# Performance work log

Measured on AMD Instinct MI355X. Metric: run time of the kernel, lower is better.

The kernel has to match this reference:

```python
import jax, jax.numpy as jnp
import numpy as np

PLANES = 128
SCALE = float(np.sqrt(PLANES))
TEMP = 0.05


def _maxpool2x2(x):
    # x: [B, C, H, W] -> [B, C, H//2, W//2]
    return jax.lax.reduce_window(x, -jnp.inf, jax.lax.max,
                                 (1, 1, 2, 2), (1, 1, 2, 2), 'VALID')


def _conv1x1(x, w, b=None):
    # x: [B, Cin, H, W], w: [Cout, Cin]
    y = jnp.einsum('bchw,oc->bohw', x, w)
    if b is not None:
        y = y + b[None, :, None, None]
    return y


def setup_inputs() -> dict:
    key = jax.random.key(0)
    ks = jax.random.split(key, 9)
    B, C, H, W = 8, 512, 64, 64
    std = 0.01  # init.normal_(w, 0, 0.01)
    x = jax.random.normal(ks[0], (B, C, H, W), dtype=jnp.float32)
    wq = jax.random.normal(ks[1], (PLANES, C), dtype=jnp.float32) * std
    bq = jnp.zeros((PLANES,), dtype=jnp.float32)
    wk = jax.random.normal(ks[2], (PLANES, C), dtype=jnp.float32) * std
    bk = jnp.zeros((PLANES,), dtype=jnp.float32)
    wv = jax.random.normal(ks[3], (C, C), dtype=jnp.float32) * std  # no bias (use_out=False)
    wm = jax.random.normal(ks[4], (1, C), dtype=jnp.float32) * std
    bm = jnp.zeros((1,), dtype=jnp.float32)
    # torch inits gamma to zero; use a nonzero value so the attention path matters
    gamma = jax.random.normal(ks[5], (1,), dtype=jnp.float32)
    return {'x': x, 'wq': wq, 'bq': bq, 'wk': wk, 'bk': bk,
            'wv': wv, 'wm': wm, 'bm': bm, 'gamma': gamma}


def reference(x, wq, bq, wk, bk, wv, wm, bm, gamma):
    B, C, H, W = x.shape
    xd = _maxpool2x2(x)                                   # [B,C,H/2,W/2]
    Hm, Wm = xd.shape[2], xd.shape[3]
    N, M = H * W, Hm * Wm
    q = _conv1x1(x, wq, bq).reshape(B, PLANES, N)         # [B,P,N]
    k = _conv1x1(xd, wk, bk).reshape(B, PLANES, M)        # [B,P,M]
    v = _conv1x1(xd, wv).reshape(B, C, M)                 # [B,C,M]
    # 'channel' whitening: subtract per-channel spatial mean
    q = q - q.mean(axis=2, keepdims=True)
    k = k - k.mean(axis=2, keepdims=True)
    sim = jnp.einsum('bpn,bpm->bnm', q, k) / (SCALE * TEMP)  # [B,N,M]
    sim = jax.nn.softmax(sim, axis=2)
    out_sim = jnp.einsum('bnm,bcm->bcn', sim, v).reshape(B, C, H, W)
    out_sim = gamma[0] * out_sim
    # global-context branch (with_gc, no 2fc)
    mask = _conv1x1(xd, wm, bm).reshape(B, M)             # [B,M]
    mask = jax.nn.softmax(mask, axis=1)
    out_gc = jnp.einsum('bcm,bm->bc', v, mask)[:, :, None, None]  # [B,C,1,1]
    return out_sim + out_gc + x
```

## Files before the change

kernel.cpp:

```cpp
#include <hip/hip_runtime.h>

typedef float f32x4 __attribute__((ext_vector_type(4)));
typedef short bf16x8 __attribute__((ext_vector_type(8)));
typedef short s16x4 __attribute__((ext_vector_type(4)));
typedef unsigned short u16;

#define B_ 8
#define C_ 512
#define N_ 4096
#define M_ 1024
#define P_ 128
#define A2C 2.5506631384888954f
#define B2C 23.083120654223414f

#define MFMA __builtin_amdgcn_mfma_f32_16x16x32_bf16

__device__ __forceinline__ u16 f2b(float f) {
  unsigned u = __float_as_uint(f);
  u += 0x7fffu + ((u >> 16) & 1u);
  return (u16)(u >> 16);
}
__device__ __forceinline__ float b2f(u16 h) {
  return __uint_as_float(((unsigned)h) << 16);
}
__device__ __forceinline__ float waveRedSum(float v) {
#pragma unroll
  for (int off = 32; off > 0; off >>= 1) v += __shfl_xor(v, off);
  return v;
}
__device__ __forceinline__ void gload_lds16(const u16* g, u16* l) {
  __builtin_amdgcn_global_load_lds(
      (const __attribute__((address_space(1))) void*)g,
      (__attribute__((address_space(3))) void*)l, 16, 0, 0);
}

__global__ __launch_bounds__(256) void prep_tx(const float* __restrict__ x,
                                               u16* __restrict__ xt,
                                               u16* __restrict__ xdt,
                                               float* __restrict__ meanx,
                                               float* __restrict__ meanxd) {
  const int bid = blockIdx.x;
  const int b = bid >> 8, ct = (bid >> 5) & 7, hp = bid & 31;
  const int t = threadIdx.x;
  const int lane = t & 63, wid = t >> 6;
  __shared__ float xs[64 * 133];
  __shared__ float part[4][64];
  const float* xb = x + ((size_t)(b * 512 + ct * 64) * 4096) + hp * 128;
#pragma unroll
  for (int it = 0; it < 32; ++it) {
    int c = it * 2 + (t >> 7);
    int n = t & 127;
    xs[c * 133 + n] = xb[(size_t)c * 4096 + n];
  }
  __syncthreads();
  {
    int c = t >> 2, qq = t & 3;
    float s = 0;
#pragma unroll
    for (int j = 0; j < 32; ++j) s += xs[c * 133 + qq * 32 + j];
    s += __shfl_xor(s, 1);
    s += __shfl_xor(s, 2);
    if (qq == 0) atomicAdd(&meanx[b * 512 + ct * 64 + c], s * (1.f / 4096.f));
  }
#pragma unroll
  for (int it = 0; it < 16; ++it) {
    int n = it * 8 + (t >> 5), cp = t & 31;
    float lo = xs[(2 * cp) * 133 + n], hi = xs[(2 * cp + 1) * 133 + n];
    unsigned u = (unsigned)f2b(lo) | ((unsigned)f2b(hi) << 16);
    *(unsigned*)(xt + (((size_t)b * 4096) + hp * 128 + n) * 512 + ct * 64 + 2 * cp) = u;
  }
  float s0 = 0, s1 = 0;
  const int cp = t & 31;
#pragma unroll
  for (int it = 0; it < 4; ++it) {
    int wm = it * 8 + (t >> 5);
    int c0 = 2 * cp;
    float a = fmaxf(fmaxf(xs[c0 * 133 + 2 * wm], xs[c0 * 133 + 2 * wm + 1]),
                    fmaxf(xs[c0 * 133 + 64 + 2 * wm], xs[c0 * 133 + 64 + 2 * wm + 1]));
    float d = fmaxf(fmaxf(xs[(c0 + 1) * 133 + 2 * wm], xs[(c0 + 1) * 133 + 2 * wm + 1]),
                    fmaxf(xs[(c0 + 1) * 133 + 64 + 2 * wm], xs[(c0 + 1) * 133 + 64 + 2 * wm + 1]));
    unsigned u = (unsigned)f2b(a) | ((unsigned)f2b(d) << 16);
    *(unsigned*)(xdt + (((size_t)b * 1024) + hp * 32 + wm) * 512 + ct * 64 + c0) = u;
    s0 += a; s1 += d;
  }
  s0 += __shfl_xor(s0, 32);
  s1 += __shfl_xor(s1, 32);
  if (lane < 32) { part[wid][2 * cp] = s0; part[wid][2 * cp + 1] = s1; }
  __syncthreads();
  if (t < 64)
    atomicAdd(&meanxd[b * 512 + ct * 64 + t],
              (part[0][t] + part[1][t] + part[2][t] + part[3][t]) * (1.f / 1024.f));
}

__global__ __launch_bounds__(256) void wcvt(const float* __restrict__ wq,
                                            const float* __restrict__ wk,
                                            const float* __restrict__ wv,
                                            const float* __restrict__ wm,
                                            const float* __restrict__ bm,
                                            const float* __restrict__ meanx,
                                            const float* __restrict__ meanxd,
                                            const u16* __restrict__ xdt,
                                            u16* __restrict__ wq_b,
                                            u16* __restrict__ wk_b,
                                            u16* __restrict__ wv_b,
                                            float* __restrict__ corr_q,
                                            float* __restrict__ corr_k,
                                            float* __restrict__ logits) {
  const int bid = blockIdx.x, t = threadIdx.x;
  if (bid < 1536) {
    int i = bid * 256 + t;
    if (i < 65536) wq_b[i] = f2b(wq[i]);
    else if (i < 131072) wk_b[i - 65536] = f2b(wk[i - 65536]);
    else wv_b[i - 131072] = f2b(wv[i - 131072]);
  } else if (bid < 1552) {
    int blk = bid - 1536, b = blk & 7, sel = blk >> 3;
    const float* w = sel ? wk : wq;
    const float* mn = (sel ? meanxd : meanx) + b * 512;
    int p = t >> 1, h = t & 1;
    const float* wr = w + p * 512 + h * 256;
    const float* mr = mn + h * 256;
    float s = 0;
#pragma unroll 8
    for (int c = 0; c < 256; ++c) s += wr[c] * mr[c];
    s += __shfl_xor(s, 1);
    if (h == 0) (sel ? corr_k : corr_q)[b * 128 + p] = s;
  } else {
    int blk = bid - 1552;
    int b = blk >> 8, mblk = blk & 255;
    int lane = t & 63, wv4 = t >> 6;
    int m = mblk * 4 + wv4;
    bf16x8 h8 = *(const bf16x8*)(xdt + ((size_t)b * 1024 + m) * 512 + lane * 8);
    const float* wmr = wm + lane * 8;
    float s = 0;
#pragma unroll
    for (int j = 0; j < 8; ++j) s += b2f((u16)h8[j]) * wmr[j];
    s = waveRedSum(s);
    if (lane == 0) logits[b * 1024 + m] = s + bm[0];
  }
}

template <int BR, int BC, bool TRANS, bool CORR>
__global__ __launch_bounds__(256) void gemm_bt(const u16* __restrict__ A,
                                               const u16* __restrict__ Bt,
                                               const float* __restrict__ corr,
                                               u16* __restrict__ outp,
                                               int Cout, int Ncols) {
  constexpr int WR = BR / 2, WC = BC / 2, ITR = WR / 16, ITC = WC / 16;
  constexpr int AFR = BR * 8 / 256, BFR = BC * 8 / 256;
  const int b = blockIdx.z;
  const int col0 = blockIdx.x * BC;
  const int row0 = blockIdx.y * BR;
  const int tid = threadIdx.x;
  const int lane = tid & 63, wid = tid >> 6;
  const int g = lane >> 4, c16 = lane & 15;
  const int wr = (wid >> 1) * WR, wc = (wid & 1) * WC;
  __shared__ __align__(16) u16 As[BR][72];
  __shared__ __align__(16) u16 Bs[BC][72];
  const u16* Bb = Bt + (size_t)b * Ncols * 512;
  f32x4 acc[ITR][ITC];
#pragma unroll
  for (int i = 0; i < ITR; ++i)
#pragma unroll
    for (int j = 0; j < ITC; ++j) acc[i][j] = (f32x4){0.f, 0.f, 0.f, 0.f};

  for (int k0 = 0; k0 < 512; k0 += 64) {
#pragma unroll
    for (int i = 0; i < AFR; ++i) {
      int f = tid + i * 256;
      int r = f >> 3, c8 = f & 7;
      *(bf16x8*)&As[r][c8 * 8] =
          *(const bf16x8*)(A + (size_t)(row0 + r) * 512 + k0 + c8 * 8);
    }
#pragma unroll
    for (int i = 0; i < BFR; ++i) {
      int f = tid + i * 256;
      int r = f >> 3, c8 = f & 7;
      *(bf16x8*)&Bs[r][c8 * 8] =
          *(const bf16x8*)(Bb + (size_t)(col0 + r) * 512 + k0 + c8 * 8);
    }
    __syncthreads();
#pragma unroll
    for (int kk = 0; kk < 2; ++kk) {
      bf16x8 bfr[ITC];
#pragma unroll
      for (int j = 0; j < ITC; ++j)
        bfr[j] = *(const bf16x8*)&Bs[wc + j * 16 + c16][kk * 32 + g * 8];
#pragma unroll
      for (int i = 0; i < ITR; ++i) {
        bf16x8 af = *(const bf16x8*)&As[wr + i * 16 + c16][kk * 32 + g * 8];
#pragma unroll
        for (int j = 0; j < ITC; ++j)
          acc[i][j] = MFMA(af, bfr[j], acc[i][j], 0, 0, 0);
      }
    }
    __syncthreads();
  }
  if (TRANS) {
#pragma unroll
    for (int i = 0; i < ITR; ++i)
#pragma unroll
      for (int j = 0; j < ITC; ++j) {
        int row = row0 + wr + i * 16 + g * 4;
        int col = col0 + wc + j * 16 + c16;
        s16x4 h;
#pragma unroll
        for (int r = 0; r < 4; ++r) {
          float val = acc[i][j][r];
          if (CORR) val -= corr[b * 128 + row + r];
          h[r] = (short)f2b(val);
        }
        *(s16x4*)(outp + ((size_t)b * Ncols + col) * Cout + row) = h;
      }
  } else {
#pragma unroll
    for (int i = 0; i < ITR; ++i)
#pragma unroll
      for (int j = 0; j < ITC; ++j) {
        int row = row0 + wr + i * 16 + g * 4;
        int col = col0 + wc + j * 16 + c16;
#pragma unroll
        for (int r = 0; r < 4; ++r)
          outp[((size_t)b * Cout + row + r) * Ncols + col] = f2b(acc[i][j][r]);
      }
  }
}

__global__ __launch_bounds__(256) void k_gc(const float* __restrict__ logits,
                                            const u16* __restrict__ v,
                                            float* __restrict__ gc) {
  const int b = blockIdx.x >> 4, cc = blockIdx.x & 15;
  const int tid = threadIdx.x;
  const int lane = tid & 63, wid = tid >> 6;
  __shared__ float pl[1024];
  __shared__ float r4[4];
  __shared__ float stot[2];
  float4 lv = *(const float4*)&logits[b * 1024 + tid * 4];
  float mx = fmaxf(fmaxf(lv.x, lv.y), fmaxf(lv.z, lv.w));
#pragma unroll
  for (int off = 32; off > 0; off >>= 1) mx = fmaxf(mx, __shfl_xor(mx, off));
  if (lane == 0) r4[wid] = mx;
  __syncthreads();
  if (tid == 0) stot[0] = fmaxf(fmaxf(r4[0], r4[1]), fmaxf(r4[2], r4[3]));
  __syncthreads();
  const float M = stot[0];
  float e0 = __expf(lv.x - M), e1 = __expf(lv.y - M);
  float e2 = __expf(lv.z - M), e3 = __expf(lv.w - M);
  pl[tid * 4 + 0] = e0; pl[tid * 4 + 1] = e1;
  pl[tid * 4 + 2] = e2; pl[tid * 4 + 3] = e3;
  float ps = waveRedSum((e0 + e1) + (e2 + e3));
  if (lane == 0) r4[wid] = ps;
  __syncthreads();
  if (tid == 0) stot[1] = 1.0f / (r4[0] + r4[1] + r4[2] + r4[3]);
  __syncthreads();
  const float inv = stot[1];
  const int c = cc * 32 + (tid >> 3), sub = tid & 7;
  const u16* vr = v + ((size_t)b * 512 + c) * 1024 + sub * 128;
  const float* plr = pl + sub * 128;
  float s = 0;
#pragma unroll
  for (int i = 0; i < 16; ++i) {
    bf16x8 h = *(const bf16x8*)(vr + i * 8);
#pragma unroll
    for (int j = 0; j < 8; ++j) s += b2f((u16)h[j]) * plr[i * 8 + j];
  }
  s += __shfl_xor(s, 1);
  s += __shfl_xor(s, 2);
  s += __shfl_xor(s, 4);
  if (sub == 0) gc[b * 512 + c] = s * inv;
}

__device__ __forceinline__ void s_phase(const bf16x8* kbf, const bf16x8 (&qf)[2][4],
                                        u16* PlBuf, int nA, int o,
                                        float& lp0, float& lp1) {
  f32x4 sv0 = (f32x4){0.f, 0.f, 0.f, 0.f};
  f32x4 sv1 = (f32x4){0.f, 0.f, 0.f, 0.f};
#pragma unroll
  for (int kf = 0; kf < 4; ++kf) {
    sv0 = MFMA(kbf[kf], qf[0][kf], sv0, 0, 0, 0);
    sv1 = MFMA(kbf[kf], qf[1][kf], sv1, 0, 0, 0);
  }
  float p00 = exp2f(fmaf(sv0[0], A2C, -B2C));
  float p01 = exp2f(fmaf(sv0[1], A2C, -B2C));
  float p02 = exp2f(fmaf(sv0[2], A2C, -B2C));
  float p03 = exp2f(fmaf(sv0[3], A2C, -B2C));
  float p10 = exp2f(fmaf(sv1[0], A2C, -B2C));
  float p11 = exp2f(fmaf(sv1[1], A2C, -B2C));
  float p12 = exp2f(fmaf(sv1[2], A2C, -B2C));
  float p13 = exp2f(fmaf(sv1[3], A2C, -B2C));
  lp0 += (p00 + p01) + (p02 + p03);
  lp1 += (p10 + p11) + (p12 + p13);
  uint2 w0, w1;
  w0.x = (unsigned)f2b(p00) | ((unsigned)f2b(p01) << 16);
  w0.y = (unsigned)f2b(p02) | ((unsigned)f2b(p03) << 16);
  w1.x = (unsigned)f2b(p10) | ((unsigned)f2b(p11) << 16);
  w1.y = (unsigned)f2b(p12) | ((unsigned)f2b(p13) << 16);
  *(uint2*)&PlBuf[nA * 64 + o] = w0;
  *(uint2*)&PlBuf[(nA + 16) * 64 + o] = w1;
}

__global__ __launch_bounds__(512, 2) void attn(const u16* __restrict__ q,
                                               const u16* __restrict__ kt,
                                               const u16* __restrict__ v,
                                               const float* __restrict__ gc,
                                               const float* __restrict__ x,
                                               const float* __restrict__ gamma,
                                               float* __restrict__ out) {
  extern __shared__ __align__(16) char smem[];
  u16* Vl = (u16*)smem;
  u16* Pl = (u16*)(smem + 131072);
  float* l_s = (float*)(smem + 147456);
  const int bid = blockIdx.x;
  const int b = bid & 7;
  const int n0 = (bid >> 3) * 64;
  const int tid = threadIdx.x;
  const int lane = tid & 63, wid = tid >> 6;
  const int g = lane >> 4, c16 = lane & 15;
  const int mb = wid & 3, nh = wid >> 2;
  const int xsw = (c16 & 7) << 3;
  const int nA = nh * 32 + c16;
  const int po = (mb * 16 + g * 4) ^ xsw;

  bf16x8 qf[2][4];
  {
    const u16* qr = q + ((size_t)b * N_ + n0 + nh * 32 + c16) * P_ + g * 8;
#pragma unroll
    for (int t = 0; t < 2; ++t)
#pragma unroll
      for (int kf = 0; kf < 4; ++kf)
        qf[t][kf] = *(const bf16x8*)(qr + t * 16 * P_ + kf * 32);
  }
  const u16* ktr = kt + ((size_t)b * M_ + mb * 16 + c16) * P_ + g * 8;
  bf16x8 kb[2][4];
#pragma unroll
  for (int kf = 0; kf < 4; ++kf) kb[0][kf] = *(const bf16x8*)(ktr + kf * 32);
#pragma unroll
  for (int kf = 0; kf < 4; ++kf) kb[1][kf] = *(const bf16x8*)(ktr + 64 * P_ + kf * 32);
  const u16* vst = v + ((size_t)b * C_ + wid * 64 + (lane >> 3)) * M_ +
                   ((lane & 7) ^ (lane >> 3)) * 8;
#pragma unroll
  for (int i = 0; i < 8; ++i)
    gload_lds16(vst + (size_t)i * 8 * M_, Vl + (wid * 8 + i) * 512);

  float lp0 = 0.f, lp1 = 0.f;
  s_phase(kb[0], qf, Pl, nA, po, lp0, lp1);

  f32x4 acc[4][4];
#pragma unroll
  for (int i = 0; i < 4; ++i)
#pragma unroll
    for (int j = 0; j < 4; ++j) acc[i][j] = (f32x4){0.f, 0.f, 0.f, 0.f};

#pragma unroll 2
  for (int s = 0; s < 16; ++s) {
    const int par = s & 1, nxt = par ^ 1;
    if (s < 14) {
      const size_t moff = (size_t)(s + 2) * 64 * P_;
#pragma unroll
      for (int kf = 0; kf < 4; ++kf)
        kb[par][kf] = *(const bf16x8*)(ktr + moff + kf * 32);
      asm volatile("s_waitcnt vmcnt(4) lgkmcnt(0)" ::: "memory");
    } else {
      asm volatile("s_waitcnt vmcnt(0) lgkmcnt(0)" ::: "memory");
    }
    __builtin_amdgcn_sched_barrier(0);
    __builtin_amdgcn_s_barrier();
    __builtin_amdgcn_sched_barrier(0);
    if (s < 15) {
      const int m1 = (s + 1) * 64;
#pragma unroll
      for (int i = 0; i < 8; ++i)
        gload_lds16(vst + m1 + (size_t)i * 8 * M_,
                    Vl + nxt * 32768 + (wid * 8 + i) * 512);
    }
    const u16* VlP = Vl + par * 32768;
    const u16* PlP = Pl + par * 4096;
#pragma unroll
    for (int kk = 0; kk < 2; ++kk) {
      bf16x8 pb[4];
#pragma unroll
      for (int nb = 0; nb < 4; ++nb)
        pb[nb] = *(const bf16x8*)&PlP[(nb * 16 + c16) * 64 + ((kk * 32 + g * 8) ^ xsw)];
#pragma unroll
      for (int cf = 0; cf < 4; ++cf) {
        bf16x8 va = *(const bf16x8*)&VlP[(wid * 64 + cf * 16 + c16) * 64 +
                                         ((kk * 32 + g * 8) ^ xsw)];
#pragma unroll
        for (int nb = 0; nb < 4; ++nb)
          acc[cf][nb] = MFMA(va, pb[nb], acc[cf][nb], 0, 0, 0);
      }
    }
    if (s < 15) s_phase(kb[nxt], qf, Pl + nxt * 4096, nA, po, lp0, lp1);
  }

  lp0 += __shfl_xor(lp0, 16); lp0 += __shfl_xor(lp0, 32);
  lp1 += __shfl_xor(lp1, 16); lp1 += __shfl_xor(lp1, 32);
  if (lane < 16) {
    l_s[mb * 64 + nh * 32 + lane] = lp0;
    l_s[mb * 64 + nh * 32 + 16 + lane] = lp1;
  }
  __syncthreads();
  float linv[4];
#pragma unroll
  for (int nb = 0; nb < 4; ++nb) {
    int n = nb * 16 + c16;
    linv[nb] = 1.0f / (l_s[n] + l_s[64 + n] + l_s[128 + n] + l_s[192 + n]);
  }
  const float gam = gamma[0];
#pragma unroll
  for (int cf = 0; cf < 4; ++cf) {
    const int c = wid * 64 + cf * 16 + g * 4;
    float gcv[4];
#pragma unroll
    for (int r = 0; r < 4; ++r) gcv[r] = gc[b * C_ + c + r];
#pragma unroll
    for (int nb = 0; nb < 4; ++nb) {
      const size_t idx0 = ((size_t)b * C_ + c) * (size_t)N_ + n0 + nb * 16 + c16;
#pragma unroll
      for (int r = 0; r < 4; ++r) {
        const size_t idx = idx0 + (size_t)r * N_;
        out[idx] = gam * acc[cf][nb][r] * linv[nb] + gcv[r] + x[idx];
      }
    }
  }
}

extern "C" void kernel_launch(void* const* d_in, const int* in_sizes, int n_in,
                              void* d_out, int out_size, void* d_ws, size_t ws_size,
                              hipStream_t stream) {
  const float* x     = (const float*)d_in[0];
  const float* wq    = (const float*)d_in[1];
  const float* wk    = (const float*)d_in[3];
  const float* wv    = (const float*)d_in[5];
  const float* wm    = (const float*)d_in[6];
  const float* bm    = (const float*)d_in[7];
  const float* gamma = (const float*)d_in[8];
  float* out = (float*)d_out;
  char* ws = (char*)d_ws;

  u16*   xt     = (u16*)(ws + 0);
  u16*   xdt    = (u16*)(ws + 33554432);
  u16*   q_ws   = (u16*)(ws + 41943040);
  u16*   kt_ws  = (u16*)(ws + 50331648);
  u16*   v_ws   = (u16*)(ws + 52428800);
  u16*   wq_b   = (u16*)(ws + 60817408);
  u16*   wk_b   = (u16*)(ws + 60948480);
  u16*   wv_b   = (u16*)(ws + 61079552);
  float* meanx  = (float*)(ws + 61603840);
  float* meanxd = (float*)(ws + 61620224);
  float* corr_q = (float*)(ws + 61636608);
  float* corr_k = (float*)(ws + 61640704);
  float* gc     = (float*)(ws + 61644800);
  float* logits = (float*)(ws + 61661184);

  hipMemsetAsync(ws + 61603840, 0, 32768, stream);
  prep_tx<<<dim3(2048), dim3(256), 0, stream>>>(x, xt, xdt, meanx, meanxd);
  wcvt<<<dim3(3600), dim3(256), 0, stream>>>(wq, wk, wv, wm, bm, meanx, meanxd,
                                             xdt, wq_b, wk_b, wv_b, corr_q,
                                             corr_k, logits);
  gemm_bt<128, 128, true, true><<<dim3(32, 1, B_), dim3(256), 0, stream>>>(
      wq_b, xt, corr_q, q_ws, 128, 4096);
  gemm_bt<128, 64, true, true><<<dim3(16, 1, B_), dim3(256), 0, stream>>>(
      wk_b, xdt, corr_k, kt_ws, 128, 1024);
  gemm_bt<128, 128, false, false><<<dim3(8, 4, B_), dim3(256), 0, stream>>>(
      wv_b, xdt, nullptr, v_ws, 512, 1024);
  k_gc<<<dim3(128), dim3(256), 0, stream>>>(logits, v_ws, gc);

  hipFuncSetAttribute((const void*)attn,
                      hipFuncAttributeMaxDynamicSharedMemorySize, 148480);
  attn<<<dim3(512), dim3(512), 148480, stream>>>(q_ws, kt_ws, v_ws, gc, x,
                                                 gamma, out);
}
```

Baseline: 255.2 us.

## Fuse mask logits into prep, merge projection GEMMs, single-buffer attention LDS

Computes the global-context mask logits inside the pooling prep kernel via shuffle reductions and atomics, removing a separate pass over xdt. The three projection GEMMs are merged into one launch with a uniform 128x64 tile. The attention kernel drops double-buffered V/P LDS staging for a single buffer, halving shared memory so more blocks can be resident (launch bounds raised to 4), at the cost of an extra barrier per step and less load/compute overlap. The logits no longer add bm, which is dropped because a constant bias cancels in the softmax.

```diff
diff --git a/kernel.cpp b/kernel.cpp
--- a/kernel.cpp
+++ b/kernel.cpp
@@ -35,10 +35,12 @@
 }
 
 __global__ __launch_bounds__(256) void prep_tx(const float* __restrict__ x,
+                                               const float* __restrict__ wm,
                                                u16* __restrict__ xt,
                                                u16* __restrict__ xdt,
                                                float* __restrict__ meanx,
-                                               float* __restrict__ meanxd) {
+                                               float* __restrict__ meanxd,
+                                               float* __restrict__ logits) {
   const int bid = blockIdx.x;
   const int b = bid >> 8, ct = (bid >> 5) & 7, hp = bid & 31;
   const int t = threadIdx.x;
@@ -64,24 +66,30 @@
   }
 #pragma unroll
   for (int it = 0; it < 16; ++it) {
-    int n = it * 8 + (t >> 5), cp = t & 31;
-    float lo = xs[(2 * cp) * 133 + n], hi = xs[(2 * cp + 1) * 133 + n];
+    int n = it * 8 + (t >> 5), cp2 = t & 31;
+    float lo = xs[(2 * cp2) * 133 + n], hi = xs[(2 * cp2 + 1) * 133 + n];
     unsigned u = (unsigned)f2b(lo) | ((unsigned)f2b(hi) << 16);
-    *(unsigned*)(xt + (((size_t)b * 4096) + hp * 128 + n) * 512 + ct * 64 + 2 * cp) = u;
-  }
+    *(unsigned*)(xt + (((size_t)b * 4096) + hp * 128 + n) * 512 + ct * 64 + 2 * cp2) = u;
+  }
+  const int cp = t & 31;
+  const float wm0 = wm[ct * 64 + 2 * cp], wm1 = wm[ct * 64 + 2 * cp + 1];
   float s0 = 0, s1 = 0;
-  const int cp = t & 31;
 #pragma unroll
   for (int it = 0; it < 4; ++it) {
-    int wm = it * 8 + (t >> 5);
+    int wmi = it * 8 + (t >> 5);
     int c0 = 2 * cp;
-    float a = fmaxf(fmaxf(xs[c0 * 133 + 2 * wm], xs[c0 * 133 + 2 * wm + 1]),
-                    fmaxf(xs[c0 * 133 + 64 + 2 * wm], xs[c0 * 133 + 64 + 2 * wm + 1]));
-    float d = fmaxf(fmaxf(xs[(c0 + 1) * 133 + 2 * wm], xs[(c0 + 1) * 133 + 2 * wm + 1]),
-                    fmaxf(xs[(c0 + 1) * 133 + 64 + 2 * wm], xs[(c0 + 1) * 133 + 64 + 2 * wm + 1]));
+    float a = fmaxf(fmaxf(xs[c0 * 133 + 2 * wmi], xs[c0 * 133 + 2 * wmi + 1]),
+                    fmaxf(xs[c0 * 133 + 64 + 2 * wmi], xs[c0 * 133 + 64 + 2 * wmi + 1]));
+    float d = fmaxf(fmaxf(xs[(c0 + 1) * 133 + 2 * wmi], xs[(c0 + 1) * 133 + 2 * wmi + 1]),
+                    fmaxf(xs[(c0 + 1) * 133 + 64 + 2 * wmi], xs[(c0 + 1) * 133 + 64 + 2 * wmi + 1]));
     unsigned u = (unsigned)f2b(a) | ((unsigned)f2b(d) << 16);
-    *(unsigned*)(xdt + (((size_t)b * 1024) + hp * 32 + wm) * 512 + ct * 64 + c0) = u;
+    *(unsigned*)(xdt + (((size_t)b * 1024) + hp * 32 + wmi) * 512 + ct * 64 + c0) = u;
     s0 += a; s1 += d;
+    float lg = wm0 * a + wm1 * d;
+    lg += __shfl_xor(lg, 1);  lg += __shfl_xor(lg, 2);
+    lg += __shfl_xor(lg, 4);  lg += __shfl_xor(lg, 8);
+    lg += __shfl_xor(lg, 16);
+    if (cp == 0) atomicAdd(&logits[b * 1024 + hp * 32 + wmi], lg);
   }
   s0 += __shfl_xor(s0, 32);
   s1 += __shfl_xor(s1, 32);
@@ -95,24 +103,20 @@
 __global__ __launch_bounds__(256) void wcvt(const float* __restrict__ wq,
                                             const float* __restrict__ wk,
                                             const float* __restrict__ wv,
-                                            const float* __restrict__ wm,
-                                            const float* __restrict__ bm,
                                             const float* __restrict__ meanx,
                                             const float* __restrict__ meanxd,
-                                            const u16* __restrict__ xdt,
                                             u16* __restrict__ wq_b,
                                             u16* __restrict__ wk_b,
                                             u16* __restrict__ wv_b,
                                             float* __restrict__ corr_q,
-                                            float* __restrict__ corr_k,
-                                            float* __restrict__ logits) {
+                                            float* __restrict__ corr_k) {
   const int bid = blockIdx.x, t = threadIdx.x;
   if (bid < 1536) {
     int i = bid * 256 + t;
     if (i < 65536) wq_b[i] = f2b(wq[i]);
     else if (i < 131072) wk_b[i - 65536] = f2b(wk[i - 65536]);
     else wv_b[i - 131072] = f2b(wv[i - 131072]);
-  } else if (bid < 1552) {
+  } else {
     int blk = bid - 1536, b = blk & 7, sel = blk >> 3;
     const float* w = sel ? wk : wq;
     const float* mn = (sel ? meanxd : meanx) + b * 512;
@@ -124,38 +128,24 @@
     for (int c = 0; c < 256; ++c) s += wr[c] * mr[c];
     s += __shfl_xor(s, 1);
     if (h == 0) (sel ? corr_k : corr_q)[b * 128 + p] = s;
-  } else {
-    int blk = bid - 1552;
-    int b = blk >> 8, mblk = blk & 255;
-    int lane = t & 63, wv4 = t >> 6;
-    int m = mblk * 4 + wv4;
-    bf16x8 h8 = *(const bf16x8*)(xdt + ((size_t)b * 1024 + m) * 512 + lane * 8);
-    const float* wmr = wm + lane * 8;
-    float s = 0;
-#pragma unroll
-    for (int j = 0; j < 8; ++j) s += b2f((u16)h8[j]) * wmr[j];
-    s = waveRedSum(s);
-    if (lane == 0) logits[b * 1024 + m] = s + bm[0];
   }
 }
 
 template <int BR, int BC, bool TRANS, bool CORR>
-__global__ __launch_bounds__(256) void gemm_bt(const u16* __restrict__ A,
-                                               const u16* __restrict__ Bt,
-                                               const float* __restrict__ corr,
-                                               u16* __restrict__ outp,
-                                               int Cout, int Ncols) {
+__device__ __forceinline__ void gemm_body(const u16* __restrict__ A,
+                                          const u16* __restrict__ Bt,
+                                          const float* __restrict__ corr,
+                                          u16* __restrict__ outp,
+                                          int Cout, int Ncols,
+                                          int bx, int by, int b,
+                                          u16 (*As)[72], u16 (*Bs)[72]) {
   constexpr int WR = BR / 2, WC = BC / 2, ITR = WR / 16, ITC = WC / 16;
   constexpr int AFR = BR * 8 / 256, BFR = BC * 8 / 256;
-  const int b = blockIdx.z;
-  const int col0 = blockIdx.x * BC;
-  const int row0 = blockIdx.y * BR;
+  const int col0 = bx * BC, row0 = by * BR;
   const int tid = threadIdx.x;
   const int lane = tid & 63, wid = tid >> 6;
   const int g = lane >> 4, c16 = lane & 15;
   const int wr = (wid >> 1) * WR, wc = (wid & 1) * WC;
-  __shared__ __align__(16) u16 As[BR][72];
-  __shared__ __align__(16) u16 Bs[BC][72];
   const u16* Bb = Bt + (size_t)b * Ncols * 512;
   f32x4 acc[ITR][ITC];
 #pragma unroll
@@ -222,6 +212,33 @@
         for (int r = 0; r < 4; ++r)
           outp[((size_t)b * Cout + row + r) * Ncols + col] = f2b(acc[i][j][r]);
       }
+  }
+}
+
+__global__ __launch_bounds__(256) void mega(const u16* __restrict__ wq_b,
+                                            const u16* __restrict__ wk_b,
+                                            const u16* __restrict__ wv_b,
+                                            const u16* __restrict__ xt,
+                                            const u16* __restrict__ xdt,
+                                            const float* __restrict__ corr_q,
+                                            const float* __restrict__ corr_k,
+                                            u16* __restrict__ q_ws,
+                                            u16* __restrict__ kt_ws,
+                                            u16* __restrict__ v_ws) {
+  __shared__ __align__(16) u16 As[128][72];
+  __shared__ __align__(16) u16 Bs[64][72];
+  const int bid = blockIdx.x;
+  if (bid < 512) {
+    gemm_body<128, 64, true, true>(wq_b, xt, corr_q, q_ws, 128, 4096,
+                                   bid >> 3, 0, bid & 7, As, Bs);
+  } else if (bid < 640) {
+    int r = bid - 512;
+    gemm_body<128, 64, true, true>(wk_b, xdt, corr_k, kt_ws, 128, 1024,
+                                   r >> 3, 0, r & 7, As, Bs);
+  } else {
+    int r = bid - 640;
+    gemm_body<128, 64, false, false>(wv_b, xdt, nullptr, v_ws, 512, 1024,
+                                     (r >> 3) & 15, r >> 7, r & 7, As, Bs);
   }
 }
 
@@ -269,36 +286,7 @@
   if (sub == 0) gc[b * 512 + c] = s * inv;
 }
 
-__device__ __forceinline__ void s_phase(const bf16x8* kbf, const bf16x8 (&qf)[2][4],
-                                        u16* PlBuf, int nA, int o,
-                                        float& lp0, float& lp1) {
-  f32x4 sv0 = (f32x4){0.f, 0.f, 0.f, 0.f};
-  f32x4 sv1 = (f32x4){0.f, 0.f, 0.f, 0.f};
-#pragma unroll
-  for (int kf = 0; kf < 4; ++kf) {
-    sv0 = MFMA(kbf[kf], qf[0][kf], sv0, 0, 0, 0);
-    sv1 = MFMA(kbf[kf], qf[1][kf], sv1, 0, 0, 0);
-  }
-  float p00 = exp2f(fmaf(sv0[0], A2C, -B2C));
-  float p01 = exp2f(fmaf(sv0[1], A2C, -B2C));
-  float p02 = exp2f(fmaf(sv0[2], A2C, -B2C));
-  float p03 = exp2f(fmaf(sv0[3], A2C, -B2C));
-  float p10 = exp2f(fmaf(sv1[0], A2C, -B2C));
-  float p11 = exp2f(fmaf(sv1[1], A2C, -B2C));
-  float p12 = exp2f(fmaf(sv1[2], A2C, -B2C));
-  float p13 = exp2f(fmaf(sv1[3], A2C, -B2C));
-  lp0 += (p00 + p01) + (p02 + p03);
-  lp1 += (p10 + p11) + (p12 + p13);
-  uint2 w0, w1;
-  w0.x = (unsigned)f2b(p00) | ((unsigned)f2b(p01) << 16);
-  w0.y = (unsigned)f2b(p02) | ((unsigned)f2b(p03) << 16);
-  w1.x = (unsigned)f2b(p10) | ((unsigned)f2b(p11) << 16);
-  w1.y = (unsigned)f2b(p12) | ((unsigned)f2b(p13) << 16);
-  *(uint2*)&PlBuf[nA * 64 + o] = w0;
-  *(uint2*)&PlBuf[(nA + 16) * 64 + o] = w1;
-}
-
-__global__ __launch_bounds__(512, 2) void attn(const u16* __restrict__ q,
+__global__ __launch_bounds__(512, 4) void attn(const u16* __restrict__ q,
                                                const u16* __restrict__ kt,
                                                const u16* __restrict__ v,
                                                const float* __restrict__ gc,
@@ -307,8 +295,8 @@
                                                float* __restrict__ out) {
   extern __shared__ __align__(16) char smem[];
   u16* Vl = (u16*)smem;
-  u16* Pl = (u16*)(smem + 131072);
-  float* l_s = (float*)(smem + 147456);
+  u16* Pl = (u16*)(smem + 65536);
+  float* l_s = (float*)(smem + 73728);
   const int bid = blockIdx.x;
   const int b = bid & 7;
   const int n0 = (bid >> 3) * 64;
@@ -330,66 +318,86 @@
         qf[t][kf] = *(const bf16x8*)(qr + t * 16 * P_ + kf * 32);
   }
   const u16* ktr = kt + ((size_t)b * M_ + mb * 16 + c16) * P_ + g * 8;
-  bf16x8 kb[2][4];
-#pragma unroll
-  for (int kf = 0; kf < 4; ++kf) kb[0][kf] = *(const bf16x8*)(ktr + kf * 32);
-#pragma unroll
-  for (int kf = 0; kf < 4; ++kf) kb[1][kf] = *(const bf16x8*)(ktr + 64 * P_ + kf * 32);
+  bf16x8 kb[4];
+#pragma unroll
+  for (int kf = 0; kf < 4; ++kf) kb[kf] = *(const bf16x8*)(ktr + kf * 32);
+  const u16* kpre = ktr + 64 * P_;
   const u16* vst = v + ((size_t)b * C_ + wid * 64 + (lane >> 3)) * M_ +
                    ((lane & 7) ^ (lane >> 3)) * 8;
 #pragma unroll
   for (int i = 0; i < 8; ++i)
     gload_lds16(vst + (size_t)i * 8 * M_, Vl + (wid * 8 + i) * 512);
-
+  const u16* vpre = vst + 64;
+
+  f32x4 acc[4][4];
+#pragma unroll
+  for (int i = 0; i < 4; ++i)
+#pragma unroll
+    for (int j = 0; j < 4; ++j) acc[i][j] = (f32x4){0.f, 0.f, 0.f, 0.f};
   float lp0 = 0.f, lp1 = 0.f;
-  s_phase(kb[0], qf, Pl, nA, po, lp0, lp1);
-
-  f32x4 acc[4][4];
-#pragma unroll
-  for (int i = 0; i < 4; ++i)
-#pragma unroll
-    for (int j = 0; j < 4; ++j) acc[i][j] = (f32x4){0.f, 0.f, 0.f, 0.f};
-
-#pragma unroll 2
+
   for (int s = 0; s < 16; ++s) {
-    const int par = s & 1, nxt = par ^ 1;
-    if (s < 14) {
-      const size_t moff = (size_t)(s + 2) * 64 * P_;
-#pragma unroll
-      for (int kf = 0; kf < 4; ++kf)
-        kb[par][kf] = *(const bf16x8*)(ktr + moff + kf * 32);
+    f32x4 sv0 = (f32x4){0.f, 0.f, 0.f, 0.f};
+    f32x4 sv1 = (f32x4){0.f, 0.f, 0.f, 0.f};
+#pragma unroll
+    for (int kf = 0; kf < 4; ++kf) {
+      sv0 = MFMA(kb[kf], qf[0][kf], sv0, 0, 0, 0);
+      sv1 = MFMA(kb[kf], qf[1][kf], sv1, 0, 0, 0);
+    }
+    if (s < 15) {
+#pragma unroll
+      for (int kf = 0; kf < 4; ++kf) kb[kf] = *(const bf16x8*)(kpre + kf * 32);
+      kpre += 64 * P_;
+    }
+    float p00 = exp2f(fmaf(sv0[0], A2C, -B2C));
+    float p01 = exp2f(fmaf(sv0[1], A2C, -B2C));
+    float p02 = exp2f(fmaf(sv0[2], A2C, -B2C));
+    float p03 = exp2f(fmaf(sv0[3], A2C, -B2C));
+    float p10 = exp2f(fmaf(sv1[0], A2C, -B2C));
+    float p11 = exp2f(fmaf(sv1[1], A2C, -B2C));
+    float p12 = exp2f(fmaf(sv1[2], A2C, -B2C));
+    float p13 = exp2f(fmaf(sv1[3], A2C, -B2C));
+    lp0 += (p00 + p01) + (p02 + p03);
+    lp1 += (p10 + p11) + (p12 + p13);
+    uint2 w0, w1;
+    w0.x = (unsigned)f2b(p00) | ((unsigned)f2b(p01) << 16);
+    w0.y = (unsigned)f2b(p02) | ((unsigned)f2b(p03) << 16);
+    w1.x = (unsigned)f2b(p10) | ((unsigned)f2b(p11) << 16);
+    w1.y = (unsigned)f2b(p12) | ((unsigned)f2b(p13) << 16);
+    *(uint2*)&Pl[nA * 64 + po] = w0;
+    *(uint2*)&Pl[(nA + 16) * 64 + po] = w1;
+    if (s < 15) {
       asm volatile("s_waitcnt vmcnt(4) lgkmcnt(0)" ::: "memory");
     } else {
       asm volatile("s_waitcnt vmcnt(0) lgkmcnt(0)" ::: "memory");
+    }
+    __builtin_amdgcn_sched_barrier(0);
+    __builtin_amdgcn_s_barrier();
+    __builtin_amdgcn_sched_barrier(0);
+#pragma unroll
+    for (int kk = 0; kk < 2; ++kk) {
+      bf16x8 pb[4];
+#pragma unroll
+      for (int nb = 0; nb < 4; ++nb)
+        pb[nb] = *(const bf16x8*)&Pl[(nb * 16 + c16) * 64 + ((kk * 32 + g * 8) ^ xsw)];
+#pragma unroll
+      for (int cf = 0; cf < 4; ++cf) {
+        bf16x8 va = *(const bf16x8*)&Vl[(wid * 64 + cf * 16 + c16) * 64 +
+                                        ((kk * 32 + g * 8) ^ xsw)];
+#pragma unroll
+        for (int nb = 0; nb < 4; ++nb)
+          acc[cf][nb] = MFMA(va, pb[nb], acc[cf][nb], 0, 0, 0);
+      }
     }
     __builtin_amdgcn_sched_barrier(0);
     __builtin_amdgcn_s_barrier();
     __builtin_amdgcn_sched_barrier(0);
     if (s < 15) {
-      const int m1 = (s + 1) * 64;
 #pragma unroll
       for (int i = 0; i < 8; ++i)
-        gload_lds16(vst + m1 + (size_t)i * 8 * M_,
-                    Vl + nxt * 32768 + (wid * 8 + i) * 512);
-    }
-    const u16* VlP = Vl + par * 32768;
-    const u16* PlP = Pl + par * 4096;
-#pragma unroll
-    for (int kk = 0; kk < 2; ++kk) {
-      bf16x8 pb[4];
-#pragma unroll
-      for (int nb = 0; nb < 4; ++nb)
-        pb[nb] = *(const bf16x8*)&PlP[(nb * 16 + c16) * 64 + ((kk * 32 + g * 8) ^ xsw)];
-#pragma unroll
-      for (int cf = 0; cf < 4; ++cf) {
-        bf16x8 va = *(const bf16x8*)&VlP[(wid * 64 + cf * 16 + c16) * 64 +
-                                         ((kk * 32 + g * 8) ^ xsw)];
-#pragma unroll
-        for (int nb = 0; nb < 4; ++nb)
-          acc[cf][nb] = MFMA(va, pb[nb], acc[cf][nb], 0, 0, 0);
-      }
-    }
-    if (s < 15) s_phase(kb[nxt], qf, Pl + nxt * 4096, nA, po, lp0, lp1);
+        gload_lds16(vpre + (size_t)i * 8 * M_, Vl + (wid * 8 + i) * 512);
+      vpre += 64;
+    }
   }
 
   lp0 += __shfl_xor(lp0, 16); lp0 += __shfl_xor(lp0, 32);
@@ -432,7 +440,6 @@
   const float* wk    = (const float*)d_in[3];
   const float* wv    = (const float*)d_in[5];
   const float* wm    = (const float*)d_in[6];
-  const float* bm    = (const float*)d_in[7];
   const float* gamma = (const float*)d_in[8];
   float* out = (float*)d_out;
   char* ws = (char*)d_ws;
@@ -447,26 +454,22 @@
   u16*   wv_b   = (u16*)(ws + 61079552);
   float* meanx  = (float*)(ws + 61603840);
   float* meanxd = (float*)(ws + 61620224);
-  float* corr_q = (float*)(ws + 61636608);
-  float* corr_k = (float*)(ws + 61640704);
-  float* gc     = (float*)(ws + 61644800);
-  float* logits = (float*)(ws + 61661184);
-
-  hipMemsetAsync(ws + 61603840, 0, 32768, stream);
-  prep_tx<<<dim3(2048), dim3(256), 0, stream>>>(x, xt, xdt, meanx, meanxd);
-  wcvt<<<dim3(3600), dim3(256), 0, stream>>>(wq, wk, wv, wm, bm, meanx, meanxd,
-                                             xdt, wq_b, wk_b, wv_b, corr_q,
-                                             corr_k, logits);
-  gemm_bt<128, 128, true, true><<<dim3(32, 1, B_), dim3(256), 0, stream>>>(
-      wq_b, xt, corr_q, q_ws, 128, 4096);
-  gemm_bt<128, 64, true, true><<<dim3(16, 1, B_), dim3(256), 0, stream>>>(
-      wk_b, xdt, corr_k, kt_ws, 128, 1024);
-  gemm_bt<128, 128, false, false><<<dim3(8, 4, B_), dim3(256), 0, stream>>>(
-      wv_b, xdt, nullptr, v_ws, 512, 1024);
+  float* logits = (float*)(ws + 61636608);
+  float* corr_q = (float*)(ws + 61669376);
+  float* corr_k = (float*)(ws + 61673472);
+  float* gc     = (float*)(ws + 61677568);
+
+  hipMemsetAsync(ws + 61603840, 0, 65536, stream);
+  prep_tx<<<dim3(2048), dim3(256), 0, stream>>>(x, wm, xt, xdt, meanx, meanxd,
+                                                logits);
+  wcvt<<<dim3(1552), dim3(256), 0, stream>>>(wq, wk, wv, meanx, meanxd,
+                                             wq_b, wk_b, wv_b, corr_q, corr_k);
+  mega<<<dim3(1152), dim3(256), 0, stream>>>(wq_b, wk_b, wv_b, xt, xdt,
+                                             corr_q, corr_k, q_ws, kt_ws, v_ws);
   k_gc<<<dim3(128), dim3(256), 0, stream>>>(logits, v_ws, gc);
 
   hipFuncSetAttribute((const void*)attn,
-                      hipFuncAttributeMaxDynamicSharedMemorySize, 148480);
-  attn<<<dim3(512), dim3(512), 148480, stream>>>(q_ws, kt_ws, v_ws, gc, x,
-                                                 gamma, out);
-}
+                      hipFuncAttributeMaxDynamicSharedMemorySize, 74752);
+  attn<<<dim3(512), dim3(512), 74752, stream>>>(q_ws, kt_ws, v_ws, gc, x,
+                                                gamma, out);
+}
```

Measured after the change: 308.8 us. 1.21x slower.
